# Kernel tuning notes

Measured on AMD Instinct MI355X. Metric: run time of the kernel, lower is better.

Reference implementation:

```python
import jax, jax.numpy as jnp
import numpy as np

N_HEADS = 16
N_KV_HEADS = 4
HEAD_DIM = 128
ROPE_THETA = 10000.0


def _rope_cos_sin(seq_len, head_dim, dtype):
    inv_freq = 1.0 / (ROPE_THETA ** (jnp.arange(0, head_dim, 2, dtype=jnp.float32) / head_dim))
    angles = jnp.arange(seq_len, dtype=jnp.float32)[:, None] * inv_freq[None, :]  # [S, hd/2]
    return jnp.cos(angles).astype(dtype), jnp.sin(angles).astype(dtype)


def _apply_rope(t, cos, sin):
    # t: [B, S, H, hd]; interleaved-pair (complex) rotation, Llama style
    B, S, H, hd = t.shape
    tr = t.reshape(B, S, H, hd // 2, 2)
    t0, t1 = tr[..., 0], tr[..., 1]
    c = cos[None, :, None, :]
    s = sin[None, :, None, :]
    out = jnp.stack([t0 * c - t1 * s, t0 * s + t1 * c], axis=-1)
    return out.reshape(B, S, H, hd)


def setup_inputs() -> dict:
    key = jax.random.key(0)
    ks = jax.random.split(key, 5)
    B, S, D = 2, 2048, 2048
    scale = 0.02
    return {
        "x": jax.random.normal(ks[0], (B, S, D), dtype=jnp.float32),
        "wq": jax.random.normal(ks[1], (N_HEADS * HEAD_DIM, D), dtype=jnp.float32) * scale,
        "wk": jax.random.normal(ks[2], (N_KV_HEADS * HEAD_DIM, D), dtype=jnp.float32) * scale,
        "wv": jax.random.normal(ks[3], (N_KV_HEADS * HEAD_DIM, D), dtype=jnp.float32) * scale,
        "wo": jax.random.normal(ks[4], (D, N_HEADS * HEAD_DIM), dtype=jnp.float32) * scale,
    }


def reference(x, wq, wk, wv, wo):
    B, S, D = x.shape
    hd = HEAD_DIM
    # QKV projections (torch Linear: y = x @ W.T)
    q = (x @ wq.T).reshape(B, S, N_HEADS, hd)
    k = (x @ wk.T).reshape(B, S, N_KV_HEADS, hd)
    v = (x @ wv.T).reshape(B, S, N_KV_HEADS, hd)
    # RoPE on q, k
    cos, sin = _rope_cos_sin(S, hd, x.dtype)
    q = _apply_rope(q, cos, sin)
    k = _apply_rope(k, cos, sin)
    # GQA: repeat kv heads to match query heads
    rep = N_HEADS // N_KV_HEADS
    k = jnp.repeat(k, rep, axis=2)  # [B, S, H, hd]
    v = jnp.repeat(v, rep, axis=2)
    # Causal SDPA
    scores = jnp.einsum("bqhd,bkhd->bhqk", q, k) / jnp.sqrt(jnp.asarray(hd, x.dtype))
    causal = jnp.tril(jnp.ones((S, S), dtype=bool))
    scores = jnp.where(causal[None, None], scores, jnp.asarray(-1e30, x.dtype))
    attn = jax.nn.softmax(scores, axis=-1)
    out = jnp.einsum("bhqk,bkhd->bqhd", attn, v).reshape(B, S, N_HEADS * hd)
    return out @ wo.T
```

## Files before the change

### kernel.cpp

```cpp
#include <hip/hip_runtime.h>
#include <stdint.h>

typedef unsigned short u16;
typedef __attribute__((ext_vector_type(8))) __bf16 bf16x8;
typedef __attribute__((ext_vector_type(4))) float f32x4;

__device__ __forceinline__ u16 f2bf(float f) {
  union { float f; uint32_t u; } v; v.f = f;
  uint32_t u = v.u;
  uint32_t r = (u + 0x7fffu + ((u >> 16) & 1u)) >> 16;
  return (u16)r;
}
__device__ __forceinline__ float bf2f(u16 h) {
  union { uint32_t u; float f; } v; v.u = ((uint32_t)h) << 16;
  return v.f;
}

__device__ __forceinline__ void gld16(const void* g, void* l) {
  __builtin_amdgcn_global_load_lds(
      (__attribute__((address_space(1))) void*)(uintptr_t)g,
      (__attribute__((address_space(3))) void*)l,
      16, 0, 0);
}

__global__ __launch_bounds__(256) void cast_all(const float* __restrict__ x,
                                                const float* __restrict__ wq,
                                                const float* __restrict__ wk,
                                                const float* __restrict__ wv,
                                                const float* __restrict__ wo,
                                                u16* __restrict__ xb,
                                                u16* __restrict__ wqkv,
                                                u16* __restrict__ wob) {
  int i = blockIdx.x * 256 + threadIdx.x;
  const float* src; u16* dst; int loc, base;
  if (i < 2097152)      { src = x;  dst = xb;   loc = i;           base = 0; }
  else if (i < 3145728) { src = wq; dst = wqkv; loc = i - 2097152; base = 0; }
  else if (i < 3407872) { src = wk; dst = wqkv; loc = i - 3145728; base = 1048576; }
  else if (i < 3670016) { src = wv; dst = wqkv; loc = i - 3407872; base = 1310720; }
  else                  { src = wo; dst = wob;  loc = i - 3670016; base = 0; }
  float4 f = ((const float4*)src)[loc];
  ushort4 o;
  o.x = f2bf(f.x); o.y = f2bf(f.y); o.z = f2bf(f.z); o.w = f2bf(f.w);
  ((ushort4*)dst)[base + loc] = o;
}

__global__ __launch_bounds__(256) void gemm_bt(const u16* __restrict__ A,
                                               const u16* __restrict__ B,
                                               void* __restrict__ C,
                                               int M, int N, int K, int out_f32)
{
  __shared__ u16 As[128 * 64];
  __shared__ u16 Bs[128 * 64];
  const int tid  = threadIdx.x;
  const int wave = tid >> 6, lane = tid & 63;
  const int col  = lane & 15, quad = lane >> 4;
  const int bm = blockIdx.y, bn = blockIdx.x;
  const int wm = (wave >> 1) * 64, wn = (wave & 1) * 64;
  const size_t arow0 = (size_t)bm * 128, brow0 = (size_t)bn * 128;

  const int sr = lane >> 3, pc = lane & 7;

  const f32x4 fz = {0.f, 0.f, 0.f, 0.f};
  f32x4 acc[4][4];
  for (int i = 0; i < 4; ++i)
    for (int j = 0; j < 4; ++j) acc[i][j] = fz;

  for (int k0 = 0; k0 < K; k0 += 64) {
    __syncthreads();
    #pragma unroll
    for (int i = 0; i < 4; ++i) {
      int rA = wave * 32 + i * 8 + sr;
      int lc = pc ^ (rA & 7);
      gld16(A + (arow0 + rA) * K + k0 + lc * 8, As + (wave * 32 + i * 8) * 64);
      gld16(B + (brow0 + rA) * K + k0 + lc * 8, Bs + (wave * 32 + i * 8) * 64);
    }
    __syncthreads();
    #pragma unroll
    for (int kk = 0; kk < 2; ++kk) {
      const int swz = (((kk * 4 + quad) ^ (col & 7)) * 8);
      bf16x8 af[4];
      #pragma unroll
      for (int mt = 0; mt < 4; ++mt)
        af[mt] = *(const bf16x8*)&As[(wm + mt * 16 + col) * 64 + swz];
      #pragma unroll
      for (int nt = 0; nt < 4; ++nt) {
        bf16x8 bf = *(const bf16x8*)&Bs[(wn + nt * 16 + col) * 64 + swz];
        #pragma unroll
        for (int mt = 0; mt < 4; ++mt)
          acc[mt][nt] = __builtin_amdgcn_mfma_f32_16x16x32_bf16(af[mt], bf, acc[mt][nt], 0, 0, 0);
      }
    }
  }

  #pragma unroll
  for (int mt = 0; mt < 4; ++mt)
    #pragma unroll
    for (int nt = 0; nt < 4; ++nt)
      #pragma unroll
      for (int i = 0; i < 4; ++i) {
        size_t grow = arow0 + wm + mt * 16 + quad * 4 + i;
        size_t gcol = brow0 + wn + nt * 16 + col;
        float v = acc[mt][nt][i];
        if (out_f32) ((float*)C)[grow * N + gcol] = v;
        else         ((u16*)C)[grow * N + gcol]   = f2bf(v);
      }
}

__global__ __launch_bounds__(256) void rope_kernel(u16* __restrict__ t, int S, float qscale) {
  int idx = blockIdx.x * 256 + threadIdx.x;
  int i = idx & 63;
  int r = idx >> 6;
  int hh = r % 20; r /= 20;
  int s = r % S;
  int b = r / S;
  float inv = exp2f(-(float)i * 0.20762050593046f);
  float ang = (float)s * inv;
  float sn, cs;
  __sincosf(ang, &sn, &cs);
  int colb = (hh < 16) ? hh * 128 : 2048 + (hh - 16) * 128;
  float osc = (hh < 16) ? qscale : 1.0f;
  size_t base = (size_t)(b * S + s) * 3072 + colb + 2 * i;
  float t0 = bf2f(t[base]), t1 = bf2f(t[base + 1]);
  t[base]     = f2bf((t0 * cs - t1 * sn) * osc);
  t[base + 1] = f2bf((t0 * sn + t1 * cs) * osc);
}

__global__ __launch_bounds__(256) void vtrans_kernel(const u16* __restrict__ qkv,
                                                     u16* __restrict__ Vtg, int S) {
  __shared__ u16 T[64 * 65];
  const int s0 = blockIdx.x * 64, d0 = blockIdx.y * 64, bk = blockIdx.z;
  const int b = bk >> 2, kvh = bk & 3;
  const u16* src = qkv + (size_t)b * S * 3072 + 2560 + kvh * 128 + d0;
  #pragma unroll 4
  for (int it = 0; it < 16; ++it) {
    int idx = it * 256 + threadIdx.x;
    int r = idx >> 6, c = idx & 63;
    T[c * 65 + r] = src[(size_t)(s0 + r) * 3072 + c];
  }
  __syncthreads();
  #pragma unroll 4
  for (int it = 0; it < 16; ++it) {
    int idx = it * 256 + threadIdx.x;
    int d = idx >> 6, s = idx & 63;
    Vtg[((size_t)bk * 128 + d0 + d) * S + s0 + s] = T[d * 65 + s];
  }
}

__global__ __launch_bounds__(256, 2) void attn_kernel(const u16* __restrict__ QKV,
                                                      const u16* __restrict__ Vtg,
                                                      u16* __restrict__ Ctx,
                                                      int B, int S)
{
  const int x = blockIdx.x;
  const int t = x >> 5, bh = x & 31;
  const int qt = (x < 256) ? (15 - t) : (t - 8);
  const int h = bh & 15, b = bh >> 4;
  const int tid  = threadIdx.x;
  const int wave = tid >> 6, lane = tid & 63;
  const int col  = lane & 15, quad = lane >> 4;
  const int q0   = qt * 128;
  const int kvh  = h >> 2;
  const int row0w = q0 + wave * 32;

  __shared__ u16 Ks[2][64 * 128];
  __shared__ u16 Vt[128 * 64];
  __shared__ u16 Ps[4][32 * 72];

  bf16x8 aq[2][4];
  #pragma unroll
  for (int mt = 0; mt < 2; ++mt)
    #pragma unroll
    for (int ks = 0; ks < 4; ++ks)
      aq[mt][ks] = *(const bf16x8*)(QKV + (size_t)(b * S + row0w + mt * 16 + col) * 3072
                                        + h * 128 + ks * 32 + quad * 8);
  #pragma unroll
  for (int mt = 0; mt < 2; ++mt)
    #pragma unroll
    for (int ks = 0; ks < 4; ++ks)
      asm volatile("" :: "v"(__builtin_bit_cast(f32x4, aq[mt][ks])));

  const u16* KVb = QKV + (size_t)b * S * 3072 + 2048 + kvh * 128;
  const u16* Vtb = Vtg + ((size_t)(b * 4 + kvh) * 128) * S;
  u16* Pw = Ps[wave];

  const f32x4 fz = {0.f, 0.f, 0.f, 0.f};
  f32x4 o[2][8];
  #pragma unroll
  for (int mt = 0; mt < 2; ++mt)
    #pragma unroll
    for (int nc = 0; nc < 8; ++nc) o[mt][nc] = fz;
  float rs[2] = {0.f, 0.f};

  const int kt_max = 2 * qt + 1;

  #pragma unroll
  for (int i = 0; i < 4; ++i) {
    int r = wave * 16 + i * 4 + (lane >> 4);
    int lc = (lane & 15) ^ (r & 15);
    gld16(KVb + (size_t)r * 3072 + lc * 8, Ks[0] + (wave * 16 + i * 4) * 128);
  }

  for (int kt = 0; kt <= kt_max; ++kt) {
    #pragma unroll
    for (int i = 0; i < 4; ++i) {
      int r = wave * 32 + i * 8 + (lane >> 3);
      int lc = (lane & 7) ^ (r & 7);
      gld16(Vtb + (size_t)r * S + kt * 64 + lc * 8, Vt + (wave * 32 + i * 8) * 64);
    }
    {
      int ktn = (kt < kt_max) ? kt + 1 : kt;
      u16* kdst = Ks[(kt + 1) & 1];
      #pragma unroll
      for (int i = 0; i < 4; ++i) {
        int r = wave * 16 + i * 4 + (lane >> 4);
        int lc = (lane & 15) ^ (r & 15);
        gld16(KVb + (size_t)(ktn * 64 + r) * 3072 + lc * 8, kdst + (wave * 16 + i * 4) * 128);
      }
    }

    asm volatile("s_waitcnt vmcnt(8)" ::: "memory");
    __builtin_amdgcn_s_barrier();

    const u16* Kc = Ks[kt & 1];
    const bool active = (kt * 64 <= row0w + 31);
    const bool need_mask = (kt * 64 + 63 > row0w);

    bf16x8 ap[2][2];
    if (active) {
      #pragma unroll
      for (int nt = 0; nt < 4; ++nt) {
        bf16x8 kA[4];
        #pragma unroll
        for (int ks = 0; ks < 4; ++ks)
          kA[ks] = *(const bf16x8*)&Kc[(nt * 16 + col) * 128 + (((ks * 4 + quad) ^ col) * 8)];
        #pragma unroll
        for (int mt = 0; mt < 2; ++mt) {
          f32x4 st = fz;
          __builtin_amdgcn_s_setprio(1);
          #pragma unroll
          for (int ks = 0; ks < 4; ++ks)
            st = __builtin_amdgcn_mfma_f32_16x16x32_bf16(kA[ks], aq[mt][ks], st, 0, 0, 0);
          __builtin_amdgcn_s_setprio(0);
          float pv[4];
          const int kbase = kt * 64 + nt * 16 + quad * 4;
          const int qrow  = row0w + mt * 16 + col;
          #pragma unroll
          for (int i = 0; i < 4; ++i) {
            float s = st[i];
            if (need_mask && (kbase + i > qrow)) s = -__builtin_inff();
            pv[i] = exp2f(s);
          }
          rs[mt] += (pv[0] + pv[1]) + (pv[2] + pv[3]);
          uint32_t d0 = (__float_as_uint(pv[0]) >> 16) | (__float_as_uint(pv[1]) & 0xffff0000u);
          uint32_t d1 = (__float_as_uint(pv[2]) >> 16) | (__float_as_uint(pv[3]) & 0xffff0000u);
          uint2 dd; dd.x = d0; dd.y = d1;
          *(uint2*)&Pw[(mt * 16 + col) * 72 + nt * 16 + quad * 4] = dd;
        }
      }
      __asm__ volatile("" ::: "memory");
      #pragma unroll
      for (int mt = 0; mt < 2; ++mt)
        #pragma unroll
        for (int ks = 0; ks < 2; ++ks)
          ap[mt][ks] = *(const bf16x8*)&Pw[(mt * 16 + col) * 72 + ks * 32 + quad * 8];
    }

    asm volatile("s_waitcnt vmcnt(4)" ::: "memory");
    __builtin_amdgcn_s_barrier();

    if (active) {
      #pragma unroll
      for (int nc = 0; nc < 8; ++nc) {
        #pragma unroll
        for (int ks = 0; ks < 2; ++ks) {
          bf16x8 bv = *(const bf16x8*)&Vt[(nc * 16 + col) * 64 + (((ks * 4 + quad) ^ (col & 7)) * 8)];
          __builtin_amdgcn_s_setprio(1);
          #pragma unroll
          for (int mt = 0; mt < 2; ++mt)
            o[mt][nc] = __builtin_amdgcn_mfma_f32_16x16x32_bf16(ap[mt][ks], bv, o[mt][nc], 0, 0, 0);
          __builtin_amdgcn_s_setprio(0);
        }
      }
    }
    __builtin_amdgcn_s_barrier();
  }

  #pragma unroll
  for (int mt = 0; mt < 2; ++mt) {
    float v = rs[mt];
    v += __shfl_xor(v, 16);
    v += __shfl_xor(v, 32);
    float lv[4];
    #pragma unroll
    for (int i = 0; i < 4; ++i)
      lv[i] = 1.0f / __shfl(v, quad * 4 + i);
    #pragma unroll
    for (int nc = 0; nc < 8; ++nc)
      #pragma unroll
      for (int i = 0; i < 4; ++i) {
        int qg = row0w + mt * 16 + quad * 4 + i;
        Ctx[(size_t)(b * S + qg) * 2048 + h * 128 + nc * 16 + col] =
            f2bf(o[mt][nc][i] * lv[i]);
      }
  }
}

extern "C" void kernel_launch(void* const* d_in, const int* in_sizes, int n_in,
                              void* d_out, int out_size, void* d_ws, size_t ws_size,
                              hipStream_t stream) {
  const int B = 2, S = 2048, D = 2048;
  const int M = B * S;
  const int NQKV = 3072;

  const float* x  = (const float*)d_in[0];
  const float* wq = (const float*)d_in[1];
  const float* wk = (const float*)d_in[2];
  const float* wv = (const float*)d_in[3];
  const float* wo = (const float*)d_in[4];

  char* ws = (char*)d_ws;
  u16* xb    = (u16*)ws; ws += (size_t)M * D * 2;
  u16* wqkvb = (u16*)ws; ws += (size_t)NQKV * D * 2;
  u16* wob   = (u16*)ws; ws += (size_t)D * D * 2;
  u16* qkvb  = (u16*)ws; ws += (size_t)M * NQKV * 2;
  u16* vtg   = (u16*)ws; ws += (size_t)B * 4 * 128 * S * 2;
  u16* ctx   = (u16*)ws; ws += (size_t)M * D * 2;

  cast_all<<<18432, 256, 0, stream>>>(x, wq, wk, wv, wo, xb, wqkvb, wob);

  gemm_bt<<<dim3(NQKV / 128, M / 128), 256, 0, stream>>>(xb, wqkvb, qkvb, M, NQKV, D, 0);

  const float qscale = 0.12751744515623627f;
  rope_kernel<<<(M * 20 * 64) / 256, 256, 0, stream>>>(qkvb, S, qscale);

  vtrans_kernel<<<dim3(S / 64, 2, B * 4), 256, 0, stream>>>(qkvb, vtg, S);

  attn_kernel<<<512, 256, 0, stream>>>(qkvb, vtg, ctx, B, S);

  gemm_bt<<<dim3(D / 128, M / 128), 256, 0, stream>>>(ctx, wob, d_out, M, D, D, 1);
}
```

Baseline: 317.0 us.

## Load V tiles directly from global into registers instead of staging through LDS

Each wave now reads its V^T fragments straight from global memory into registers at the start of each active tile, and the shared Vt buffer and its async global-to-LDS staging are removed. The K prefetch is skipped on the last iteration, and the three per-iteration barriers with manual vmcnt waits become a single __syncthreads. This frees LDS and removes barriers and staging traffic. In exchange, every wave issues its own uncoalesced strided global loads of V (the four waves share a KV head, so V is fetched redundantly), and those loads are exposed on the critical path with no prefetch, while register pressure rises from the 16 bf16x8 fragments.

```diff
diff --git a/kernel.cpp b/kernel.cpp
--- a/kernel.cpp
+++ b/kernel.cpp
@@ -163,7 +163,6 @@
   const int row0w = q0 + wave * 32;
 
   __shared__ u16 Ks[2][64 * 128];
-  __shared__ u16 Vt[128 * 64];
   __shared__ u16 Ps[4][32 * 72];
 
   bf16x8 aq[2][4];
@@ -199,34 +198,33 @@
     int lc = (lane & 15) ^ (r & 15);
     gld16(KVb + (size_t)r * 3072 + lc * 8, Ks[0] + (wave * 16 + i * 4) * 128);
   }
+  __syncthreads();
 
   for (int kt = 0; kt <= kt_max; ++kt) {
-    #pragma unroll
-    for (int i = 0; i < 4; ++i) {
-      int r = wave * 32 + i * 8 + (lane >> 3);
-      int lc = (lane & 7) ^ (r & 7);
-      gld16(Vtb + (size_t)r * S + kt * 64 + lc * 8, Vt + (wave * 32 + i * 8) * 64);
-    }
-    {
-      int ktn = (kt < kt_max) ? kt + 1 : kt;
+    if (kt < kt_max) {
       u16* kdst = Ks[(kt + 1) & 1];
       #pragma unroll
       for (int i = 0; i < 4; ++i) {
         int r = wave * 16 + i * 4 + (lane >> 4);
         int lc = (lane & 15) ^ (r & 15);
-        gld16(KVb + (size_t)(ktn * 64 + r) * 3072 + lc * 8, kdst + (wave * 16 + i * 4) * 128);
+        gld16(KVb + (size_t)((kt + 1) * 64 + r) * 3072 + lc * 8,
+              kdst + (wave * 16 + i * 4) * 128);
       }
     }
 
-    asm volatile("s_waitcnt vmcnt(8)" ::: "memory");
-    __builtin_amdgcn_s_barrier();
-
-    const u16* Kc = Ks[kt & 1];
     const bool active = (kt * 64 <= row0w + 31);
-    const bool need_mask = (kt * 64 + 63 > row0w);
-
-    bf16x8 ap[2][2];
     if (active) {
+      const bool need_mask = (kt * 64 + 63 > row0w);
+      const u16* Kc = Ks[kt & 1];
+
+      bf16x8 bv[8][2];
+      #pragma unroll
+      for (int nc = 0; nc < 8; ++nc)
+        #pragma unroll
+        for (int ks = 0; ks < 2; ++ks)
+          bv[nc][ks] = *(const bf16x8*)(Vtb + (size_t)(nc * 16 + col) * S
+                                            + kt * 64 + (ks * 4 + quad) * 8);
+
       #pragma unroll
       for (int nt = 0; nt < 4; ++nt) {
         bf16x8 kA[4];
@@ -258,31 +256,27 @@
         }
       }
       __asm__ volatile("" ::: "memory");
+
+      bf16x8 ap[2][2];
       #pragma unroll
       for (int mt = 0; mt < 2; ++mt)
         #pragma unroll
         for (int ks = 0; ks < 2; ++ks)
           ap[mt][ks] = *(const bf16x8*)&Pw[(mt * 16 + col) * 72 + ks * 32 + quad * 8];
-    }
-
-    asm volatile("s_waitcnt vmcnt(4)" ::: "memory");
-    __builtin_amdgcn_s_barrier();
-
-    if (active) {
       #pragma unroll
       for (int nc = 0; nc < 8; ++nc) {
         #pragma unroll
         for (int ks = 0; ks < 2; ++ks) {
-          bf16x8 bv = *(const bf16x8*)&Vt[(nc * 16 + col) * 64 + (((ks * 4 + quad) ^ (col & 7)) * 8)];
           __builtin_amdgcn_s_setprio(1);
           #pragma unroll
           for (int mt = 0; mt < 2; ++mt)
-            o[mt][nc] = __builtin_amdgcn_mfma_f32_16x16x32_bf16(ap[mt][ks], bv, o[mt][nc], 0, 0, 0);
+            o[mt][nc] = __builtin_amdgcn_mfma_f32_16x16x32_bf16(ap[mt][ks], bv[nc][ks], o[mt][nc], 0, 0, 0);
           __builtin_amdgcn_s_setprio(0);
         }
       }
     }
-    __builtin_amdgcn_s_barrier();
+
+    __syncthreads();
   }
 
   #pragma unroll
```

After: 347.4 us. 9.6% more time.
